# Optimization experiments

Measured on AMD Instinct MI355X. Metric: run time of the kernel, lower is better.

The kernel has to match this reference:

```python
import jax, jax.numpy as jnp
import numpy as np

B, LQ, LK, H = 8, 2048, 2048, 1024


def setup_inputs() -> dict:
    key = jax.random.key(0)
    kq, kk, kv, km, kw = jax.random.split(key, 5)
    input_Q = jax.random.normal(kq, (B, LQ, H), dtype=jnp.float32)
    input_K = jax.random.normal(kk, (B, LK, H), dtype=jnp.float32)
    input_V = jax.random.normal(kv, (B, LK, H), dtype=jnp.float32)
    mask = jax.random.randint(km, (B, LK), 0, 2, dtype=jnp.int32)
    # learned parameter w_omega [H, H]; scaled init so scores are O(1)-ish
    w_omega = jax.random.normal(kw, (H, H), dtype=jnp.float32) * (H ** -0.5)
    return {"input_Q": input_Q, "input_K": input_K, "input_V": input_V,
            "w_omega": w_omega, "mask": mask}


def reference(input_Q, input_K, input_V, w_omega, mask):
    # att_input = Q @ W : [B, Lq, H]
    att_input = jnp.einsum('bqh,hd->bqd', input_Q, w_omega)
    # scores = att_input @ K^T : [B, Lq, Lk]
    att_scores = jnp.einsum('bqd,bkd->bqk', att_input, input_K)
    # masked fill with -inf where mask == 0 (mask broadcast over query dim)
    neg_inf = jnp.asarray(-jnp.inf, dtype=att_scores.dtype)
    scores = jnp.where(mask[:, None, :] == 0, neg_inf, att_scores)
    probs_softmax = jax.nn.softmax(scores, axis=-1)          # [B, Lq, Lk]
    probs_sigmoid = jax.nn.sigmoid(scores)                   # sigmoid(-inf)=0
    probs_sigmoid_hat = (probs_sigmoid > 0.5).astype(probs_softmax.dtype)
    att_output_softmax = jnp.einsum('bqk,bkh->bqh', probs_softmax, input_V)
    att_output_sigmoid = jnp.einsum('bqk,bkh->bqh', probs_sigmoid_hat, input_V)
    # torch .squeeze(1) is a no-op here since Lq > 1
    return (att_output_softmax, att_output_sigmoid, probs_softmax, probs_sigmoid)
```

## Files before the change

### kernel.cpp

```cpp
#include <hip/hip_runtime.h>
#include <math.h>

#define B_  8
#define LQ_ 2048
#define LK_ 2048
#define H_  1024

#define TAU      4e-3f
#define FIX_CAP  32768
#define FIX_E    8
#define SCL      256.0f
#define SCLQ     16.0f
#define INV_SS   (1.0f / 1048576.0f)

#define KBLK 512

typedef unsigned short ushort_t;
typedef __attribute__((ext_vector_type(8))) _Float16 v8h;
typedef __attribute__((ext_vector_type(8))) short  v8s;
typedef __attribute__((ext_vector_type(4))) float  v4f;
typedef __attribute__((ext_vector_type(4))) float  f4;
typedef __attribute__((ext_vector_type(4))) int    i4;
typedef __attribute__((ext_vector_type(4))) short  s4;

#if defined(__has_builtin)
#if __has_builtin(__builtin_amdgcn_global_load_lds)
#define HAS_GLDS 1
#endif
#endif

__device__ __forceinline__ ushort_t f2bf(float x) {
  unsigned u = __float_as_uint(x);
  u = (u + 0x7FFFu + ((u >> 16) & 1u)) >> 16;
  return (ushort_t)u;
}
__device__ __forceinline__ void split2h(float x, ushort_t& h, ushort_t& l) {
  union { _Float16 f; ushort_t u; } a, b;
  a.f = (_Float16)x;
  b.f = (_Float16)(x - (float)a.f);
  h = a.u; l = b.u;
}

__device__ __forceinline__ void gld_lds16(void* lds_dst, const void* g_src) {
#ifdef HAS_GLDS
  __builtin_amdgcn_global_load_lds((const __attribute__((address_space(1))) void*)g_src,
                                   (__attribute__((address_space(3))) void*)lds_dst,
                                   16, 0, 0);
#else
  *(i4*)lds_dst = *(const i4*)g_src;
#endif
}

__device__ __forceinline__ void xcd_remap(int& bx, int& by, int& bz) {
  const int nx = gridDim.x, ny = gridDim.y;
  const int nwg = nx * ny * gridDim.z;
  const int hwid = bx + nx * (by + ny * bz);
  const int work = (hwid & 7) * (nwg >> 3) + (hwid >> 3);
  bx = work % nx;
  const int t = work / nx;
  by = t % ny;
  bz = t / ny;
}

#define WAIT_VM(n) asm volatile("s_waitcnt vmcnt(" #n ")" ::: "memory")
#define WAIT_LGKM0() do { asm volatile("s_waitcnt lgkmcnt(0)" ::: "memory"); \
                          __builtin_amdgcn_sched_barrier(0); } while (0)

__global__ void k_zero(int* p) { *p = 0; }

__global__ void k_split(const float* __restrict__ x, ushort_t* __restrict__ hi,
                        ushort_t* __restrict__ lo, int n4, float scale) {
  int stride = gridDim.x * blockDim.x;
  for (int i = blockIdx.x * blockDim.x + threadIdx.x; i < n4; i += stride) {
    f4 v = ((const f4*)x)[i];
    s4 h, l;
#pragma unroll
    for (int j = 0; j < 4; j++) {
      ushort_t hb, lb; split2h(v[j] * scale, hb, lb);
      h[j] = (short)hb; l[j] = (short)lb;
    }
    ((s4*)hi)[i] = h;
    ((s4*)lo)[i] = l;
  }
}

template <int SPLIT>
__global__ void k_transpose(const float* __restrict__ X, ushort_t* __restrict__ Yhi,
                            ushort_t* __restrict__ Ylo, int R, int C, float scale) {
  __shared__ float t[32][33];
  const int b = blockIdx.z;
  const float* Xb = X + (size_t)b * R * C;
  ushort_t* Yh = Yhi + (size_t)b * R * C;
  const int c0 = blockIdx.x * 32, r0 = blockIdx.y * 32;
  const int tx = threadIdx.x, ty = threadIdx.y;
#pragma unroll
  for (int i = 0; i < 4; i++)
    t[ty + 8 * i][tx] = Xb[(size_t)(r0 + ty + 8 * i) * C + c0 + tx];
  __syncthreads();
#pragma unroll
  for (int i = 0; i < 4; i++) {
    float v = t[tx][ty + 8 * i] * scale;
    size_t o = (size_t)(c0 + ty + 8 * i) * R + r0 + tx;
    if (SPLIT) {
      ushort_t h, l; split2h(v, h, l);
      Yh[o] = h;
      (Ylo + (size_t)b * R * C)[o] = l;
    } else {
      Yh[o] = f2bf(v);
    }
  }
}


template <int EPI>
__global__ __launch_bounds__(512, 1)
void gemm_hx2p(const ushort_t* __restrict__ Ahi, const ushort_t* __restrict__ Alo,
               const ushort_t* __restrict__ Bhi, const ushort_t* __restrict__ Blo,
               int KD, long strideAB, long strideBB, int N,
               ushort_t* __restrict__ OutHi, ushort_t* __restrict__ OutLo, long strideOB,
               float* __restrict__ S, float* __restrict__ G, ushort_t* __restrict__ Hatb,
               const int* __restrict__ mask, int* __restrict__ cnt, int* __restrict__ flist) {
  int bx = blockIdx.x, by = blockIdx.y, bz = blockIdx.z;
  xcd_remap(bx, by, bz);
  const int b  = bz;
  const int m0 = by * 128;
  const int n0 = bx * 256;
  const ushort_t* Ah = Ahi + (size_t)b * strideAB + (size_t)m0 * KD;
  const ushort_t* Al = Alo + (size_t)b * strideAB + (size_t)m0 * KD;
  const ushort_t* Bh = Bhi + (size_t)b * strideBB + (size_t)n0 * KD;
  const ushort_t* Bl = Blo + (size_t)b * strideBB + (size_t)n0 * KD;

  __shared__ __attribute__((aligned(16))) char lds[3 * 49152];

  const int tid  = threadIdx.x;
  const int lane = tid & 63;
  const int w    = tid >> 6;
  const int wm   = (w >> 2) * 64;
  const int wn   = (w & 3) * 64;
  const int fr   = lane & 15;
  const int cq   = lane >> 4;

  v4f acc[4][4] = {};

  const int r4 = tid >> 2;
  const int gc = (tid & 3) ^ ((r4 >> 1) & 3);
  const size_t goA  = (size_t)r4 * KD + gc * 8;
  const size_t goB1 = (size_t)(r4 + 128) * KD + gc * 8;
  const int lo16 = tid * 16;

#define STG_HX(t_) do {                                                  \
    char* sb = lds + ((t_) % 3) * 49152;                                 \
    const int kk = (t_) * 32;                                            \
    gld_lds16(sb + lo16,                 Ah + goA  + kk);                \
    gld_lds16(sb + 8192 + lo16,          Al + goA  + kk);                \
    gld_lds16(sb + 16384 + lo16,         Bh + goA  + kk);                \
    gld_lds16(sb + 24576 + lo16,         Bh + goB1 + kk);                \
    gld_lds16(sb + 32768 + lo16,         Bl + goA  + kk);                \
    gld_lds16(sb + 40960 + lo16,         Bl + goB1 + kk);                \
  } while (0)

  const int nT = KD / 32;
  STG_HX(0);
  STG_HX(1);
  for (int t = 0; t < nT; ++t) {
    if (t + 1 < nT) WAIT_VM(6);
    else            WAIT_VM(0);
    __builtin_amdgcn_s_barrier();

    const char* sb = lds + (t % 3) * 49152;
    v8h a_h[4], a_l[4], b_h[4], b_l[4];
#pragma unroll
    for (int i = 0; i < 4; i++) {
      const int Ra = wm + i * 16 + fr;
      const int oa = Ra * 64 + ((cq ^ ((Ra >> 1) & 3)) << 4);
      a_h[i] = *(const v8h*)(sb + oa);
      a_l[i] = *(const v8h*)(sb + 8192 + oa);
      const int Rb = wn + i * 16 + fr;
      const int ob = Rb * 64 + ((cq ^ ((Rb >> 1) & 3)) << 4);
      b_h[i] = *(const v8h*)(sb + 16384 + ob);
      b_l[i] = *(const v8h*)(sb + 32768 + ob);
    }
    if (t + 2 < nT) STG_HX(t + 2);

    WAIT_LGKM0();
    __builtin_amdgcn_s_setprio(1);
#pragma unroll
    for (int i = 0; i < 4; i++)
#pragma unroll
      for (int j = 0; j < 4; j++) {
        acc[i][j] = __builtin_amdgcn_mfma_f32_16x16x32_f16(a_h[i], b_h[j], acc[i][j], 0, 0, 0);
        acc[i][j] = __builtin_amdgcn_mfma_f32_16x16x32_f16(a_h[i], b_l[j], acc[i][j], 0, 0, 0);
        acc[i][j] = __builtin_amdgcn_mfma_f32_16x16x32_f16(a_l[i], b_h[j], acc[i][j], 0, 0, 0);
      }
    __builtin_amdgcn_s_setprio(0);
  }
#undef STG_HX

  const int rg = (lane >> 4) * 4;
#pragma unroll
  for (int i = 0; i < 4; i++)
#pragma unroll
    for (int j = 0; j < 4; j++)
#pragma unroll
      for (int r = 0; r < 4; r++) {
        const int grow = m0 + wm + i * 16 + rg + r;
        const int gcol = n0 + wn + j * 16 + fr;
        const float v = acc[i][j][r];
        if (EPI == 0) {
          size_t o = (size_t)b * strideOB + (size_t)grow * N + gcol;
          ushort_t h, l; split2h(v, h, l);
          OutHi[o] = h; OutLo[o] = l;
        } else {
          size_t o = ((size_t)b * LQ_ + grow) * N + gcol;
          const float sv = v * INV_SS;
          S[o] = sv;
          int mk = mask[b * N + gcol];
          const float g = mk ? 1.0f / (1.0f + expf(-sv)) : 0.0f;
          G[o] = g;
          Hatb[o] = (g > 0.5f) ? (ushort_t)0x3F80 : (ushort_t)0;
          if (mk && fabsf(sv) < TAU) {
            int idx = atomicAdd(cnt, 1);
            if (idx < FIX_CAP) flist[idx] = (b << 22) | (grow << 11) | gcol;
          }
        }
      }
}

__global__ __launch_bounds__(256)
void k_fix_blas(const int* __restrict__ cnt, const int* __restrict__ flist,
                const float* __restrict__ Q, const float* __restrict__ Kx,
                const float* __restrict__ W, float* __restrict__ S,
                float* __restrict__ G, ushort_t* __restrict__ Hatb) {
  const int n = min(*cnt, FIX_CAP);
  const int base = blockIdx.x * FIX_E;
  if (base >= n) return;
  const int ne = min(FIX_E, n - base);
  const int tid = threadIdx.x;

  __shared__ float qs[FIX_E][H_];
  __shared__ float aA[FIX_E][H_];
  __shared__ int   ent[FIX_E];

  if (tid < FIX_E) ent[tid] = flist[base + ((tid < ne) ? tid : 0)];
  __syncthreads();

  for (int e = 0; e < FIX_E; e++) {
    const int en = ent[e];
    const int b = en >> 22, q = (en >> 11) & 2047;
    const float* Qr = Q + ((size_t)b * LQ_ + q) * H_;
    for (int i = tid; i < H_; i += 256) qs[e][i] = Qr[i];
  }
  __syncthreads();

  float atot[FIX_E][4];
  float acc[FIX_E][4];
  const float* Wp = W + tid * 4;
#pragma unroll
  for (int blk = 0; blk < 2; blk++) {
    const int h0 = blk * KBLK;
    const int h1 = h0 + KBLK;
#pragma unroll
    for (int e = 0; e < FIX_E; e++)
#pragma unroll
      for (int j = 0; j < 4; j++) acc[e][j] = 0.f;
    for (int h = h0; h < h1; h++) {
      f4 w = *(const f4*)(Wp + (size_t)h * H_);
#pragma unroll
      for (int e = 0; e < FIX_E; e++) {
        const float qv = qs[e][h];
        acc[e][0] = fmaf(qv, w[0], acc[e][0]);
        acc[e][1] = fmaf(qv, w[1], acc[e][1]);
        acc[e][2] = fmaf(qv, w[2], acc[e][2]);
        acc[e][3] = fmaf(qv, w[3], acc[e][3]);
      }
    }
#pragma unroll
    for (int e = 0; e < FIX_E; e++)
#pragma unroll
      for (int j = 0; j < 4; j++)
        atot[e][j] = (blk == 0) ? acc[e][j] : __fadd_rn(atot[e][j], acc[e][j]);
  }
#pragma unroll
  for (int e = 0; e < FIX_E; e++) {
    aA[e][tid * 4 + 0] = atot[e][0];
    aA[e][tid * 4 + 1] = atot[e][1];
    aA[e][tid * 4 + 2] = atot[e][2];
    aA[e][tid * 4 + 3] = atot[e][3];
  }
  __syncthreads();

  if (tid < ne) {
    const int e = tid;
    const int en = ent[e];
    const int b = en >> 22, q = (en >> 11) & 2047, k = en & 2047;
    const float* Kr = Kx + ((size_t)b * LK_ + k) * H_;
    const float* Ar = aA[e];
    float stot = 0.f;
#pragma unroll
    for (int blk = 0; blk < 2; blk++) {
      const int d0 = blk * KBLK;
      const int d1 = d0 + KBLK;
      float a = 0.f;
#pragma unroll 16
      for (int d = d0; d < d1; d++) a = fmaf(Ar[d], Kr[d], a);
      stot = (blk == 0) ? a : __fadd_rn(stot, a);
    }
    size_t o = ((size_t)b * LQ_ + q) * LK_ + k;
    S[o] = stot;
    const float g = 1.0f / (1.0f + expf(-stot));
    G[o] = g;
    Hatb[o] = (g > 0.5f) ? (ushort_t)0x3F80 : (ushort_t)0;
  }
}

__global__ void k_softmax(float* __restrict__ S, const int* __restrict__ mask,
                          ushort_t* __restrict__ Pb) {
  const int row = blockIdx.x;
  const int b   = row >> 11;
  float* Sr = S + (size_t)row * LK_;
  const int* mr = mask + b * LK_;
  const int tid = threadIdx.x;
  const int c0 = tid * 8;

  float v[8]; int mk[8];
  f4 v0 = *(const f4*)&Sr[c0];
  f4 v1 = *(const f4*)&Sr[c0 + 4];
  i4 m0 = *(const i4*)&mr[c0];
  i4 m1 = *(const i4*)&mr[c0 + 4];
#pragma unroll
  for (int j = 0; j < 4; j++) { v[j] = v0[j]; v[4 + j] = v1[j]; mk[j] = m0[j]; mk[4 + j] = m1[j]; }

  float mx = -INFINITY;
#pragma unroll
  for (int j = 0; j < 8; j++) if (mk[j]) mx = fmaxf(mx, v[j]);
#pragma unroll
  for (int off = 32; off; off >>= 1) mx = fmaxf(mx, __shfl_xor(mx, off));
  __shared__ float redm[4], reds[4];
  const int lane = tid & 63, wid = tid >> 6;
  if (lane == 0) redm[wid] = mx;
  __syncthreads();
  mx = fmaxf(fmaxf(redm[0], redm[1]), fmaxf(redm[2], redm[3]));

  float e[8], sum = 0.f;
#pragma unroll
  for (int j = 0; j < 8; j++) { e[j] = mk[j] ? expf(v[j] - mx) : 0.f; sum += e[j]; }
#pragma unroll
  for (int off = 32; off; off >>= 1) sum += __shfl_xor(sum, off);
  if (lane == 0) reds[wid] = sum;
  __syncthreads();
  sum = reds[0] + reds[1] + reds[2] + reds[3];
  const float inv = 1.0f / sum;

  f4 o0, o1;
  v8s pb;
#pragma unroll
  for (int j = 0; j < 4; j++) {
    o0[j] = e[j] * inv; o1[j] = e[4 + j] * inv;
    pb[j] = (short)f2bf(o0[j]); pb[4 + j] = (short)f2bf(o1[j]);
  }
  *(f4*)&Sr[c0] = o0;
  *(f4*)&Sr[c0 + 4] = o1;
  *(v8s*)&Pb[(size_t)row * LK_ + c0] = pb;
}

__global__ __launch_bounds__(512, 1)
void gemm_pv2p(const ushort_t* __restrict__ P, const ushort_t* __restrict__ Hb,
               const ushort_t* __restrict__ Bt,
               float* __restrict__ O0, float* __restrict__ O1) {
  int bx = blockIdx.x, by = blockIdx.y, bz = blockIdx.z;
  xcd_remap(bx, by, bz);
  const int b  = bz;
  const int m0 = by * 128;
  const int n0 = bx * 256;
  const ushort_t* Pa = P  + ((size_t)b * LQ_ + m0) * (size_t)LK_;
  const ushort_t* Ha = Hb + ((size_t)b * LQ_ + m0) * (size_t)LK_;
  const ushort_t* Bb = Bt + ((size_t)b * H_  + n0) * (size_t)LK_;

  __shared__ __attribute__((aligned(16))) char lds[3 * 32768];

  const int tid  = threadIdx.x;
  const int lane = tid & 63;
  const int w    = tid >> 6;
  const int wm   = (w >> 2) * 64;
  const int wn   = (w & 3) * 64;
  const int fr   = lane & 15;
  const int cq   = lane >> 4;

  v4f acc0[4][4] = {}, acc1[4][4] = {};

  const int r4 = tid >> 2;
  const int gc = (tid & 3) ^ ((r4 >> 1) & 3);
  const size_t goA  = (size_t)r4 * LK_ + gc * 8;
  const size_t goB1 = (size_t)(r4 + 128) * LK_ + gc * 8;
  const int lo16 = tid * 16;

#define STG_PV(t_) do {                                                  \
    char* sb = lds + ((t_) % 3) * 32768;                                 \
    const int kk = (t_) * 32;                                            \
    gld_lds16(sb + lo16,          Pa + goA  + kk);                       \
    gld_lds16(sb + 8192 + lo16,   Ha + goA  + kk);                       \
    gld_lds16(sb + 16384 + lo16,  Bb + goA  + kk);                       \
    gld_lds16(sb + 24576 + lo16,  Bb + goB1 + kk);                       \
  } while (0)

  const int nT = LK_ / 32;
  STG_PV(0);
  STG_PV(1);
  for (int t = 0; t < nT; ++t) {
    if (t + 1 < nT) WAIT_VM(4);
    else            WAIT_VM(0);
    __builtin_amdgcn_s_barrier();

    const char* sb = lds + (t % 3) * 32768;
    v8s pf[4], hf[4], bf[4];
#pragma unroll
    for (int i = 0; i < 4; i++) {
      const int Ra = wm + i * 16 + fr;
      const int oa = Ra * 64 + ((cq ^ ((Ra >> 1) & 3)) << 4);
      pf[i] = *(const v8s*)(sb + oa);
      hf[i] = *(const v8s*)(sb + 8192 + oa);
      const int Rb = wn + i * 16 + fr;
      bf[i] = *(const v8s*)(sb + 16384 + Rb * 64 + ((cq ^ ((Rb >> 1) & 3)) << 4));
    }
    if (t + 2 < nT) STG_PV(t + 2);

    WAIT_LGKM0();
    __builtin_amdgcn_s_setprio(1);
#pragma unroll
    for (int i = 0; i < 4; i++)
#pragma unroll
      for (int j = 0; j < 4; j++) {
        acc0[i][j] = __builtin_amdgcn_mfma_f32_16x16x32_bf16(pf[i], bf[j], acc0[i][j], 0, 0, 0);
        acc1[i][j] = __builtin_amdgcn_mfma_f32_16x16x32_bf16(hf[i], bf[j], acc1[i][j], 0, 0, 0);
      }
    __builtin_amdgcn_s_setprio(0);
  }
#undef STG_PV

  const int rg = (lane >> 4) * 4;
#pragma unroll
  for (int i = 0; i < 4; i++)
#pragma unroll
    for (int j = 0; j < 4; j++)
#pragma unroll
      for (int r = 0; r < 4; r++) {
        const int grow = m0 + wm + i * 16 + rg + r;
        const int gcol = n0 + wn + j * 16 + fr;
        const size_t o = ((size_t)b * LQ_ + grow) * H_ + gcol;
        O0[o] = acc0[i][j][r];
        O1[o] = acc1[i][j][r];
      }
}

extern "C" void kernel_launch(void* const* d_in, const int* in_sizes, int n_in,
                              void* d_out, int out_size, void* d_ws, size_t ws_size,
                              hipStream_t stream) {
  const float* Q = (const float*)d_in[0];
  const float* K = (const float*)d_in[1];
  const float* V = (const float*)d_in[2];
  const float* W = (const float*)d_in[3];
  const int* mask = (const int*)d_in[4];

  float* out0 = (float*)d_out;
  float* out1 = out0 + (size_t)B_ * LQ_ * H_;
  float* out2 = out1 + (size_t)B_ * LQ_ * H_;
  float* out3 = out2 + (size_t)B_ * LQ_ * LK_;

  const size_t NQ = (size_t)B_ * LQ_ * H_;
  char* ws = (char*)d_ws;
  int* cnt   = (int*)ws;                    ws += 256;
  int* flist = (int*)ws;                    ws += FIX_CAP * 4;
  ushort_t* Qhi = (ushort_t*)ws;            ws += NQ * 2;
  ushort_t* Qlo = (ushort_t*)ws;            ws += NQ * 2;
  ushort_t* Khi = (ushort_t*)ws;            ws += NQ * 2;
  ushort_t* Klo = (ushort_t*)ws;            ws += NQ * 2;
  ushort_t* Ahi = (ushort_t*)ws;            ws += NQ * 2;
  ushort_t* Alo = (ushort_t*)ws;            ws += NQ * 2;
  ushort_t* Vt  = (ushort_t*)ws;            ws += NQ * 2;
  ushort_t* Wthi = (ushort_t*)ws;           ws += (size_t)H_ * H_ * 2;
  ushort_t* Wtlo = (ushort_t*)ws;

  ushort_t* hatb = Qhi;
  ushort_t* Pb   = Ahi;

  k_zero<<<1, 1, 0, stream>>>(cnt);

  k_split<<<2048, 256, 0, stream>>>(Q, Qhi, Qlo, (int)(NQ / 4), SCLQ);
  k_split<<<2048, 256, 0, stream>>>(K, Khi, Klo, (int)(NQ / 4), SCL);
  dim3 tb(32, 8);
  k_transpose<1><<<dim3(32, 32, 1), tb, 0, stream>>>(W, Wthi, Wtlo, H_, H_, SCL);
  k_transpose<0><<<dim3(32, 64, B_), tb, 0, stream>>>(V, Vt, nullptr, LK_, H_, 1.0f);

  gemm_hx2p<0><<<dim3(H_ / 256, LQ_ / 128, B_), 512, 0, stream>>>(
      Qhi, Qlo, Wthi, Wtlo, H_, (long)LQ_ * H_, 0L, H_,
      Ahi, Alo, (long)LQ_ * H_, nullptr, nullptr, nullptr, nullptr, nullptr, nullptr);

  gemm_hx2p<1><<<dim3(LK_ / 256, LQ_ / 128, B_), 512, 0, stream>>>(
      Ahi, Alo, Khi, Klo, H_, (long)LQ_ * H_, (long)LK_ * H_, LK_,
      nullptr, nullptr, 0L, out2, out3, hatb, mask, cnt, flist);

  k_fix_blas<<<FIX_CAP / FIX_E, 256, 0, stream>>>(cnt, flist, Q, K, W, out2, out3, hatb);

  k_softmax<<<B_ * LQ_, 256, 0, stream>>>(out2, mask, Pb);

  gemm_pv2p<<<dim3(H_ / 256, LQ_ / 128, B_), 512, 0, stream>>>(Pb, hatb, Vt, out0, out1);
}
```

Before: 850.7 us.

## Enlarge hx2p GEMM tile to 256x256 with double-buffered LDS pipeline

Doubles the M tile of the split-precision GEMM from 128 to 256 rows, so each wave computes 8x4 accumulator blocks and reuses the B fragments across twice as many A rows, halving grid size. The LDS pipeline changes from triple-buffered with two stages in flight to double-buffered with one stage prefetched and a full vmcnt(0) wait each iteration, and A fragments are now loaded inside the MFMA loop. The explicit lgkmcnt wait with sched barrier is removed in both GEMMs and left to the compiler. This raises register pressure (128 accumulator vectors) and reduces latency hiding and grid parallelism in exchange for better operand reuse.

```diff
diff --git a/kernel.cpp b/kernel.cpp
--- a/kernel.cpp
+++ b/kernel.cpp
@@ -63,8 +63,6 @@
 }
 
 #define WAIT_VM(n) asm volatile("s_waitcnt vmcnt(" #n ")" ::: "memory")
-#define WAIT_LGKM0() do { asm volatile("s_waitcnt lgkmcnt(0)" ::: "memory"); \
-                          __builtin_amdgcn_sched_barrier(0); } while (0)
 
 __global__ void k_zero(int* p) { *p = 0; }
 
@@ -123,82 +121,81 @@
   int bx = blockIdx.x, by = blockIdx.y, bz = blockIdx.z;
   xcd_remap(bx, by, bz);
   const int b  = bz;
-  const int m0 = by * 128;
+  const int m0 = by * 256;
   const int n0 = bx * 256;
   const ushort_t* Ah = Ahi + (size_t)b * strideAB + (size_t)m0 * KD;
   const ushort_t* Al = Alo + (size_t)b * strideAB + (size_t)m0 * KD;
   const ushort_t* Bh = Bhi + (size_t)b * strideBB + (size_t)n0 * KD;
   const ushort_t* Bl = Blo + (size_t)b * strideBB + (size_t)n0 * KD;
 
-  __shared__ __attribute__((aligned(16))) char lds[3 * 49152];
+  __shared__ __attribute__((aligned(16))) char lds[2 * 65536];
 
   const int tid  = threadIdx.x;
   const int lane = tid & 63;
   const int w    = tid >> 6;
-  const int wm   = (w >> 2) * 64;
+  const int wm   = (w >> 2) * 128;
   const int wn   = (w & 3) * 64;
   const int fr   = lane & 15;
   const int cq   = lane >> 4;
 
-  v4f acc[4][4] = {};
+  v4f acc[8][4] = {};
 
   const int r4 = tid >> 2;
   const int gc = (tid & 3) ^ ((r4 >> 1) & 3);
-  const size_t goA  = (size_t)r4 * KD + gc * 8;
-  const size_t goB1 = (size_t)(r4 + 128) * KD + gc * 8;
+  const size_t go1 = (size_t)r4 * KD + gc * 8;
+  const size_t go2 = (size_t)(r4 + 128) * KD + gc * 8;
   const int lo16 = tid * 16;
 
 #define STG_HX(t_) do {                                                  \
-    char* sb = lds + ((t_) % 3) * 49152;                                 \
+    char* sb = lds + ((t_) & 1) * 65536;                                 \
     const int kk = (t_) * 32;                                            \
-    gld_lds16(sb + lo16,                 Ah + goA  + kk);                \
-    gld_lds16(sb + 8192 + lo16,          Al + goA  + kk);                \
-    gld_lds16(sb + 16384 + lo16,         Bh + goA  + kk);                \
-    gld_lds16(sb + 24576 + lo16,         Bh + goB1 + kk);                \
-    gld_lds16(sb + 32768 + lo16,         Bl + goA  + kk);                \
-    gld_lds16(sb + 40960 + lo16,         Bl + goB1 + kk);                \
+    gld_lds16(sb + lo16,          Ah + go1 + kk);                        \
+    gld_lds16(sb + 8192  + lo16,  Ah + go2 + kk);                        \
+    gld_lds16(sb + 16384 + lo16,  Al + go1 + kk);                        \
+    gld_lds16(sb + 24576 + lo16,  Al + go2 + kk);                        \
+    gld_lds16(sb + 32768 + lo16,  Bh + go1 + kk);                        \
+    gld_lds16(sb + 40960 + lo16,  Bh + go2 + kk);                        \
+    gld_lds16(sb + 49152 + lo16,  Bl + go1 + kk);                        \
+    gld_lds16(sb + 57344 + lo16,  Bl + go2 + kk);                        \
   } while (0)
 
   const int nT = KD / 32;
   STG_HX(0);
-  STG_HX(1);
   for (int t = 0; t < nT; ++t) {
-    if (t + 1 < nT) WAIT_VM(6);
-    else            WAIT_VM(0);
+    WAIT_VM(0);
     __builtin_amdgcn_s_barrier();
-
-    const char* sb = lds + (t % 3) * 49152;
-    v8h a_h[4], a_l[4], b_h[4], b_l[4];
-#pragma unroll
-    for (int i = 0; i < 4; i++) {
+    if (t + 1 < nT) STG_HX(t + 1);
+
+    const char* sb = lds + (t & 1) * 65536;
+    v8h b_h[4], b_l[4];
+#pragma unroll
+    for (int j = 0; j < 4; j++) {
+      const int Rb = wn + j * 16 + fr;
+      const int ob = Rb * 64 + ((cq ^ ((Rb >> 1) & 3)) << 4);
+      b_h[j] = *(const v8h*)(sb + 32768 + ob);
+      b_l[j] = *(const v8h*)(sb + 49152 + ob);
+    }
+    __builtin_amdgcn_s_setprio(1);
+#pragma unroll
+    for (int i = 0; i < 8; i++) {
       const int Ra = wm + i * 16 + fr;
       const int oa = Ra * 64 + ((cq ^ ((Ra >> 1) & 3)) << 4);
-      a_h[i] = *(const v8h*)(sb + oa);
-      a_l[i] = *(const v8h*)(sb + 8192 + oa);
-      const int Rb = wn + i * 16 + fr;
-      const int ob = Rb * 64 + ((cq ^ ((Rb >> 1) & 3)) << 4);
-      b_h[i] = *(const v8h*)(sb + 16384 + ob);
-      b_l[i] = *(const v8h*)(sb + 32768 + ob);
-    }
-    if (t + 2 < nT) STG_HX(t + 2);
-
-    WAIT_LGKM0();
-    __builtin_amdgcn_s_setprio(1);
-#pragma unroll
-    for (int i = 0; i < 4; i++)
+      v8h a_h = *(const v8h*)(sb + oa);
+      v8h a_l = *(const v8h*)(sb + 16384 + oa);
 #pragma unroll
       for (int j = 0; j < 4; j++) {
-        acc[i][j] = __builtin_amdgcn_mfma_f32_16x16x32_f16(a_h[i], b_h[j], acc[i][j], 0, 0, 0);
-        acc[i][j] = __builtin_amdgcn_mfma_f32_16x16x32_f16(a_h[i], b_l[j], acc[i][j], 0, 0, 0);
-        acc[i][j] = __builtin_amdgcn_mfma_f32_16x16x32_f16(a_l[i], b_h[j], acc[i][j], 0, 0, 0);
+        acc[i][j] = __builtin_amdgcn_mfma_f32_16x16x32_f16(a_h, b_h[j], acc[i][j], 0, 0, 0);
+        acc[i][j] = __builtin_amdgcn_mfma_f32_16x16x32_f16(a_h, b_l[j], acc[i][j], 0, 0, 0);
+        acc[i][j] = __builtin_amdgcn_mfma_f32_16x16x32_f16(a_l, b_h[j], acc[i][j], 0, 0, 0);
       }
+    }
     __builtin_amdgcn_s_setprio(0);
   }
 #undef STG_HX
 
   const int rg = (lane >> 4) * 4;
 #pragma unroll
-  for (int i = 0; i < 4; i++)
+  for (int i = 0; i < 8; i++)
 #pragma unroll
     for (int j = 0; j < 4; j++)
 #pragma unroll
@@ -424,7 +421,6 @@
     }
     if (t + 2 < nT) STG_PV(t + 2);
 
-    WAIT_LGKM0();
     __builtin_amdgcn_s_setprio(1);
 #pragma unroll
     for (int i = 0; i < 4; i++)
@@ -491,11 +487,11 @@
   k_transpose<1><<<dim3(32, 32, 1), tb, 0, stream>>>(W, Wthi, Wtlo, H_, H_, SCL);
   k_transpose<0><<<dim3(32, 64, B_), tb, 0, stream>>>(V, Vt, nullptr, LK_, H_, 1.0f);
 
-  gemm_hx2p<0><<<dim3(H_ / 256, LQ_ / 128, B_), 512, 0, stream>>>(
+  gemm_hx2p<0><<<dim3(H_ / 256, LQ_ / 256, B_), 512, 0, stream>>>(
       Qhi, Qlo, Wthi, Wtlo, H_, (long)LQ_ * H_, 0L, H_,
       Ahi, Alo, (long)LQ_ * H_, nullptr, nullptr, nullptr, nullptr, nullptr, nullptr);
 
-  gemm_hx2p<1><<<dim3(LK_ / 256, LQ_ / 128, B_), 512, 0, stream>>>(
+  gemm_hx2p<1><<<dim3(LK_ / 256, LQ_ / 256, B_), 512, 0, stream>>>(
       Ahi, Alo, Khi, Klo, H_, (long)LQ_ * H_, (long)LK_ * H_, LK_,
       nullptr, nullptr, 0L, out2, out3, hatb, mask, cnt, flist);
 
```

Result: no change. 847.6 us (-0.4%).
